# Kernel optimization log

Measured on AMD Instinct MI355X. Metric: run time of the kernel, lower is better.

Reference implementation:

```python
import jax, jax.numpy as jnp
import numpy as np

B = 8192
EPS = 1e-5

def _bn(x):
    # BatchNorm1d(affine=False) in training mode: batch mean, biased variance
    m = x.mean(axis=0)
    v = x.var(axis=0)
    return (x - m) / jnp.sqrt(v + EPS)

def setup_inputs() -> dict:
    key = jax.random.key(0)
    ks = jax.random.split(key, 16)
    sparse_feat = jax.random.randint(ks[0], (B, 26), 0, 1000, dtype=jnp.int32)
    dense_feat = jax.random.normal(ks[1], (B, 13), dtype=jnp.float32)
    emb_a = jax.random.normal(ks[2], (8, 100000, 106), dtype=jnp.float32)
    emb_b = jax.random.normal(ks[3], (10, 10000, 60), dtype=jnp.float32)
    emb_c = jax.random.normal(ks[4], (8, 1000, 33), dtype=jnp.float32)
    F = 8 * 106 + 10 * 60 + 8 * 33 + 13  # 1725
    n_cross = 4  # n_cross_layer + 1
    cross_w = jax.random.normal(ks[5], (n_cross, F), dtype=jnp.float32)
    cross_b = jax.random.normal(ks[6], (n_cross, F), dtype=jnp.float32)
    s = 1.0 / np.sqrt(F)
    W1 = jax.random.uniform(ks[7], (F, 1024), minval=-s, maxval=s, dtype=jnp.float32)
    b1 = jax.random.uniform(ks[8], (1024,), minval=-s, maxval=s, dtype=jnp.float32)
    s = 1.0 / np.sqrt(1024)
    W2 = jax.random.uniform(ks[9], (1024, 512), minval=-s, maxval=s, dtype=jnp.float32)
    b2 = jax.random.uniform(ks[10], (512,), minval=-s, maxval=s, dtype=jnp.float32)
    s = 1.0 / np.sqrt(512)
    W3 = jax.random.uniform(ks[11], (512, 256), minval=-s, maxval=s, dtype=jnp.float32)
    b3 = jax.random.uniform(ks[12], (256,), minval=-s, maxval=s, dtype=jnp.float32)
    s = 1.0 / np.sqrt(F + 256)
    Wout = jax.random.uniform(ks[13], (F + 256, 1), minval=-s, maxval=s, dtype=jnp.float32)
    return {"sparse_feat": sparse_feat, "dense_feat": dense_feat,
            "emb_a": emb_a, "emb_b": emb_b, "emb_c": emb_c,
            "cross_w": cross_w, "cross_b": cross_b,
            "W1": W1, "b1": b1, "W2": W2, "b2": b2, "W3": W3, "b3": b3,
            "Wout": Wout}

def reference(sparse_feat, dense_feat, emb_a, emb_b, emb_c,
              cross_w, cross_b, W1, b1, W2, b2, W3, b3, Wout):
    # multi-embedding gather + concat
    ia = sparse_feat[:, :8]          # (B,8)
    ib = sparse_feat[:, 8:18]        # (B,10)
    ic = sparse_feat[:, 18:26]       # (B,8)
    va = emb_a[jnp.arange(8)[None, :], ia].reshape(ia.shape[0], -1)    # (B, 8*106)
    vb = emb_b[jnp.arange(10)[None, :], ib].reshape(ib.shape[0], -1)   # (B, 10*60)
    vc = emb_c[jnp.arange(8)[None, :], ic].reshape(ic.shape[0], -1)    # (B, 8*33)
    h = jnp.concatenate([va, vb, vc, dense_feat], axis=1)              # (B, F)
    h = _bn(h)
    # CrossNetwork: x_{i+1} = x0 * (x_i . w_i) + b_i + x_i
    # (matmul(x0, x_i^T) @ w_i == x0 * dot(x_i, w_i), same math, O(F) form)
    x0 = h
    xi = h
    for i in range(cross_w.shape[0]):
        xi = x0 * (xi @ cross_w[i])[:, None] + cross_b[i][None, :] + xi
    out_cross = xi                                                     # (B, F)
    # DeepNetwork: Linear -> BN(affine=False) -> ReLU, three layers
    d = jax.nn.relu(_bn(h @ W1 + b1))
    d = jax.nn.relu(_bn(d @ W2 + b2))
    d = jax.nn.relu(_bn(d @ W3 + b3))                                  # (B, 256)
    final = jnp.concatenate([out_cross, d], axis=1)                    # (B, F+256)
    logits = (final @ Wout)[:, 0]
    return jax.nn.sigmoid(logits)
```

## Files before the change

kernel.cpp:

```cpp
#include <hip/hip_runtime.h>
#include <math.h>

#define B 8192
#define FA 848
#define FB 600
#define FC 264
#define ND 13
#define F 1725
#define KP1 1728
#define N1 1024
#define N2 512
#define N3 256
#define EPS 1e-5f

typedef __attribute__((ext_vector_type(4))) float f32x4;
typedef __attribute__((ext_vector_type(8))) short bf16x8;
typedef unsigned short u16;
typedef unsigned int u32;

__device__ __forceinline__ u16 f2bf(float x) {
  u32 b = __builtin_bit_cast(u32, x);
  u32 r = (b + 0x7fffu + ((b >> 16) & 1u)) >> 16;
  return (u16)r;
}
__device__ __forceinline__ float bf2f(u16 h) {
  return __builtin_bit_cast(float, (u32)h << 16);
}

__global__ __launch_bounds__(256) void gather_kernel(
    const int* __restrict__ sparse, const float* __restrict__ dense,
    const float* __restrict__ ea, const float* __restrict__ eb,
    const float* __restrict__ ec, float* __restrict__ h) {
  int r = blockIdx.x;
  const int* sp = sparse + r * 26;
  float* hr = h + (size_t)r * F;
  for (int j = threadIdx.x; j < F; j += 256) {
    float v;
    if (j < FA) {
      int t = j / 106, c = j - t * 106;
      v = ea[(size_t)t * 10600000 + (size_t)sp[t] * 106 + c];
    } else if (j < FA + FB) {
      int jj = j - FA; int t = jj / 60, c = jj - t * 60;
      v = eb[(size_t)t * 600000 + (size_t)sp[8 + t] * 60 + c];
    } else if (j < FA + FB + FC) {
      int jj = j - FA - FB; int t = jj / 33, c = jj - t * 33;
      v = ec[(size_t)t * 33000 + (size_t)sp[18 + t] * 33 + c];
    } else {
      v = dense[r * ND + (j - (FA + FB + FC))];
    }
    hr[j] = v;
  }
}

__global__ __launch_bounds__(256) void colstat_kernel(
    const float* __restrict__ X, int C, float* __restrict__ sums) {
  int j = blockIdx.x * 256 + threadIdx.x;
  if (j >= C) return;
  int rows_per = B / gridDim.y;
  int r0 = blockIdx.y * rows_per;
  int r1 = r0 + rows_per;
  float s = 0.f, ss = 0.f;
  for (int r = r0; r < r1; ++r) {
    float x = X[(size_t)r * C + j];
    s += x; ss += x * x;
  }
  atomicAdd(&sums[j], s);
  atomicAdd(&sums[C + j], ss);
}

__global__ __launch_bounds__(256) void finstat_kernel(
    const float* __restrict__ sums, int C, float* __restrict__ mi) {
  int j = blockIdx.x * 256 + threadIdx.x;
  if (j >= C) return;
  float m = sums[j] * (1.0f / B);
  float v = sums[C + j] * (1.0f / B) - m * m;
  mi[j] = m;
  mi[C + j] = rsqrtf(v + EPS);
}

__global__ __launch_bounds__(256) void bnapply_h_kernel(
    const float* __restrict__ h, const float* __restrict__ mi,
    u32* __restrict__ hbf) {
  int r = blockIdx.x;
  const float* xr = h + (size_t)r * F;
  u32* br = hbf + (size_t)r * (KP1 / 2);
  for (int jj = threadIdx.x; jj < KP1 / 2; jj += 256) {
    int c0 = jj * 2, c1 = c0 + 1;
    float x0 = 0.f, x1 = 0.f;
    if (c0 < F) x0 = (xr[c0] - mi[c0]) * mi[F + c0];
    if (c1 < F) x1 = (xr[c1] - mi[c1]) * mi[F + c1];
    br[jj] = (u32)f2bf(x0) | ((u32)f2bf(x1) << 16);
  }
}

__global__ __launch_bounds__(256) void prep_kernel(
    const float* __restrict__ mi, const float* __restrict__ cw,
    const float* __restrict__ cb, const float* __restrict__ wout,
    float* __restrict__ cwf, float* __restrict__ consts) {
  int tid = threadIdx.x;
  float acc9[9];
#pragma unroll
  for (int q = 0; q < 9; ++q) acc9[q] = 0.f;
  for (int j = tid; j < F; j += 256) {
    float m = mi[j], inv = mi[F + j];
    float w0 = cw[j], w1 = cw[F + j], w2 = cw[2 * F + j], w3 = cw[3 * F + j];
    float w4 = wout[j];
    cwf[j] = inv * w0;          acc9[0] += m * inv * w0;
    cwf[F + j] = inv * w1;      acc9[1] += m * inv * w1;
    cwf[2 * F + j] = inv * w2;  acc9[2] += m * inv * w2;
    cwf[3 * F + j] = inv * w3;  acc9[3] += m * inv * w3;
    cwf[4 * F + j] = inv * w4;  acc9[4] += m * inv * w4;
    float c1 = cb[j];
    float c2 = c1 + cb[F + j];
    float c3 = c2 + cb[2 * F + j];
    float c4 = c3 + cb[3 * F + j];
    acc9[5] += c1 * w1;
    acc9[6] += c2 * w2;
    acc9[7] += c3 * w3;
    acc9[8] += c4 * w4;
  }
  __shared__ float red[9][4];
  int lane = tid & 63, wid = tid >> 6;
#pragma unroll
  for (int q = 0; q < 9; ++q) {
    float v = acc9[q];
    for (int off = 32; off; off >>= 1) v += __shfl_down(v, off, 64);
    if (lane == 0) red[q][wid] = v;
  }
  __syncthreads();
  if (tid == 0) {
    float t[9];
#pragma unroll
    for (int q = 0; q < 9; ++q) t[q] = red[q][0] + red[q][1] + red[q][2] + red[q][3];
    consts[0] = t[0]; consts[1] = t[1]; consts[2] = t[2]; consts[3] = t[3];
    consts[4] = t[4];
    consts[5] = 0.f; consts[6] = t[5]; consts[7] = t[6]; consts[8] = t[7];
    consts[9] = t[8];
  }
}

__global__ __launch_bounds__(256) void gemv_cross_kernel(
    const float* __restrict__ h, const float* __restrict__ cwf,
    const float* __restrict__ consts, float* __restrict__ cpart) {
  int r = blockIdx.x, tid = threadIdx.x;
  const float* hr = h + (size_t)r * F;
  float p[5] = {0.f, 0.f, 0.f, 0.f, 0.f};
  for (int j = tid; j < F; j += 256) {
    float x = hr[j];
    p[0] += x * cwf[j];
    p[1] += x * cwf[F + j];
    p[2] += x * cwf[2 * F + j];
    p[3] += x * cwf[3 * F + j];
    p[4] += x * cwf[4 * F + j];
  }
  __shared__ float red[5][4];
  int lane = tid & 63, wid = tid >> 6;
#pragma unroll
  for (int i = 0; i < 5; ++i) {
    float v = p[i];
    for (int off = 32; off; off >>= 1) v += __shfl_down(v, off, 64);
    if (lane == 0) red[i][wid] = v;
  }
  __syncthreads();
  if (tid == 0) {
    float u[5];
#pragma unroll
    for (int i = 0; i < 5; ++i)
      u[i] = red[i][0] + red[i][1] + red[i][2] + red[i][3] - consts[i];
    float a = 1.f;
#pragma unroll
    for (int i = 0; i < 4; ++i) {
      float s = a * u[i] + consts[5 + i];
      a += s;
    }
    cpart[r] = a * u[4] + consts[9];
  }
}

__global__ __launch_bounds__(256) void convw_kernel(
    const float* __restrict__ W, int K, int N, int Kp, u16* __restrict__ Wt) {
  __shared__ float t[32][33];
  int n0 = blockIdx.x * 32, k0 = blockIdx.y * 32;
  int tx = threadIdx.x, ty = threadIdx.y;
#pragma unroll
  for (int i = 0; i < 4; ++i) {
    int k = k0 + ty + i * 8;
    t[ty + i * 8][tx] = (k < K) ? W[(size_t)k * N + n0 + tx] : 0.f;
  }
  __syncthreads();
#pragma unroll
  for (int i = 0; i < 4; ++i) {
    int n = n0 + ty + i * 8;
    Wt[(size_t)n * Kp + k0 + tx] = f2bf(t[tx][ty + i * 8]);
  }
}

template <bool OUT_BF>
__global__ __launch_bounds__(256) void gemm_bf16_kernel(
    const u16* __restrict__ A, const u16* __restrict__ Bt,
    void* __restrict__ Cout, float* __restrict__ gsum, int N, int K) {
  __shared__ u16 As[128 * 32];
  __shared__ u16 Bs[128 * 32];
  int tid = threadIdx.x;
  int lane = tid & 63;
  int wave = tid >> 6;
  int row0 = blockIdx.y * 128, col0 = blockIdx.x * 128;
  int wm = (wave >> 1) * 64, wn = (wave & 1) * 64;
  int mrow = lane & 15;
  int kq = lane >> 4;

  f32x4 acc[4][4];
#pragma unroll
  for (int i = 0; i < 4; ++i)
#pragma unroll
    for (int j = 0; j < 4; ++j) acc[i][j] = (f32x4){0.f, 0.f, 0.f, 0.f};

  int kc = (tid & 3) * 8;
  const u16* Ag = A + (size_t)row0 * K;
  const u16* Bg = Bt + (size_t)col0 * K;

  for (int k0 = 0; k0 < K; k0 += 32) {
#pragma unroll
    for (int i = 0; i < 2; ++i) {
      int u = i * 256 + tid;
      int rr = u >> 2;
      __builtin_amdgcn_global_load_lds(
          (const __attribute__((address_space(1))) u32*)(Ag + (size_t)rr * K + k0 + kc),
          (__attribute__((address_space(3))) u32*)(As + u * 8), 16, 0, 0);
      __builtin_amdgcn_global_load_lds(
          (const __attribute__((address_space(1))) u32*)(Bg + (size_t)rr * K + k0 + kc),
          (__attribute__((address_space(3))) u32*)(Bs + u * 8), 16, 0, 0);
    }
    __syncthreads();
    bf16x8 af[4], bfr[4];
#pragma unroll
    for (int mi = 0; mi < 4; ++mi)
      af[mi] = *(const bf16x8*)(As + (wm + mi * 16 + mrow) * 32 + kq * 8);
#pragma unroll
    for (int ni = 0; ni < 4; ++ni)
      bfr[ni] = *(const bf16x8*)(Bs + (wn + ni * 16 + mrow) * 32 + kq * 8);
#pragma unroll
    for (int mi = 0; mi < 4; ++mi)
#pragma unroll
      for (int ni = 0; ni < 4; ++ni)
        acc[mi][ni] = __builtin_amdgcn_mfma_f32_16x16x32_bf16(
            af[mi], bfr[ni], acc[mi][ni], 0, 0, 0);
    __syncthreads();
  }

  float* sred = (float*)As;
  sred[tid] = 0.f;
  __syncthreads();
#pragma unroll
  for (int ni = 0; ni < 4; ++ni) {
    int col_l = wn + ni * 16 + mrow;
    int col = col0 + col_l;
    float s = 0.f, ss = 0.f;
#pragma unroll
    for (int mi = 0; mi < 4; ++mi) {
#pragma unroll
      for (int reg = 0; reg < 4; ++reg) {
        int row = row0 + wm + mi * 16 + kq * 4 + reg;
        float v = acc[mi][ni][reg];
        if (OUT_BF) {
          u16 hb = f2bf(v);
          v = bf2f(hb);
          ((u16*)Cout)[(size_t)row * N + col] = hb;
        } else {
          ((float*)Cout)[(size_t)row * N + col] = v;
        }
        s += v;
        ss += v * v;
      }
    }
    s += __shfl_xor(s, 16, 64);  s += __shfl_xor(s, 32, 64);
    ss += __shfl_xor(ss, 16, 64); ss += __shfl_xor(ss, 32, 64);
    if (kq == 0) {
      atomicAdd(&sred[col_l], s);
      atomicAdd(&sred[128 + col_l], ss);
    }
  }
  __syncthreads();
  if (tid < 128) {
    atomicAdd(&gsum[col0 + tid], sred[tid]);
    atomicAdd(&gsum[N + col0 + tid], sred[128 + tid]);
  }
}

__global__ __launch_bounds__(256) void bn_relu_bb_kernel(
    const uint4* __restrict__ X, const float* __restrict__ mi,
    uint4* __restrict__ out, int Cmask, int total8) {
  int i = blockIdx.x * 256 + threadIdx.x;
  if (i >= total8) return;
  uint4 v = X[i];
  int colb = (i << 3) & Cmask;
  int C = Cmask + 1;
  u32 w[4] = {v.x, v.y, v.z, v.w};
  u32 o[4];
#pragma unroll
  for (int e = 0; e < 4; ++e) {
    int c0 = colb + e * 2, c1 = c0 + 1;
    float x0 = bf2f((u16)(w[e] & 0xffffu));
    float x1 = bf2f((u16)(w[e] >> 16));
    x0 = fmaxf((x0 - mi[c0]) * mi[C + c0], 0.f);
    x1 = fmaxf((x1 - mi[c1]) * mi[C + c1], 0.f);
    o[e] = (u32)f2bf(x0) | ((u32)f2bf(x1) << 16);
  }
  out[i] = make_uint4(o[0], o[1], o[2], o[3]);
}

__global__ __launch_bounds__(256) void bn_relu_f32_kernel(
    float* __restrict__ X, int C, const float* __restrict__ mi) {
  int r = blockIdx.x;
  float* xr = X + (size_t)r * C;
  for (int j = threadIdx.x; j < C; j += 256) {
    float x = (xr[j] - mi[j]) * mi[C + j];
    xr[j] = fmaxf(x, 0.f);
  }
}

__global__ __launch_bounds__(256) void final_kernel(
    const float* __restrict__ cpart, const float* __restrict__ d3,
    const float* __restrict__ wout, float* __restrict__ out) {
  int r = blockIdx.x, tid = threadIdx.x;
  float local = d3[(size_t)r * N3 + tid] * wout[F + tid];
  for (int off = 32; off; off >>= 1) local += __shfl_down(local, off, 64);
  __shared__ float red[4];
  int lane = tid & 63, wid = tid >> 6;
  if (lane == 0) red[wid] = local;
  __syncthreads();
  if (tid == 0) {
    float s = cpart[r] + red[0] + red[1] + red[2] + red[3];
    out[r] = 1.0f / (1.0f + expf(-s));
  }
}

extern "C" void kernel_launch(void* const* d_in, const int* in_sizes, int n_in,
                              void* d_out, int out_size, void* d_ws,
                              size_t ws_size, hipStream_t stream) {
  const int* sparse = (const int*)d_in[0];
  const float* dense = (const float*)d_in[1];
  const float* ea = (const float*)d_in[2];
  const float* eb = (const float*)d_in[3];
  const float* ec = (const float*)d_in[4];
  const float* cw = (const float*)d_in[5];
  const float* cb = (const float*)d_in[6];
  const float* W1 = (const float*)d_in[7];
  const float* W2 = (const float*)d_in[9];
  const float* W3 = (const float*)d_in[11];
  const float* Wout = (const float*)d_in[13];
  float* out = (float*)d_out;

  float* ws = (float*)d_ws;
  size_t o = 0;
  float* h = ws + o;      o += (size_t)B * F;
  float* z3 = ws + o;     o += (size_t)B * N3;
  float* cpart = ws + o;  o += B;
  float* sums = ws + o;   o += 4096;
  float* mi = ws + o;     o += 4096;
  float* consts = ws + o; o += 16;
  float* cwf = ws + o;    o += 5 * F + 8;  o = (o + 7) & ~(size_t)7;
  u16* hbf = (u16*)(ws + o);  o += (size_t)B * KP1 / 2;
  u16* z1 = (u16*)(ws + o);   o += (size_t)B * N1 / 2;
  u16* z1n = (u16*)(ws + o);  o += (size_t)B * N1 / 2;
  u16* z2 = (u16*)(ws + o);   o += (size_t)B * N2 / 2;
  u16* z2n = (u16*)(ws + o);  o += (size_t)B * N2 / 2;
  u16* W1t = (u16*)(ws + o);  o += (size_t)N1 * KP1 / 2;
  u16* W2t = (u16*)(ws + o);  o += (size_t)N2 * N1 / 2;
  u16* W3t = (u16*)(ws + o);  o += (size_t)N3 * N2 / 2;

  dim3 tb(32, 8);
  convw_kernel<<<dim3(N1 / 32, KP1 / 32), tb, 0, stream>>>(W1, F, N1, KP1, W1t);
  convw_kernel<<<dim3(N2 / 32, N1 / 32), tb, 0, stream>>>(W2, N1, N2, N1, W2t);
  convw_kernel<<<dim3(N3 / 32, N2 / 32), tb, 0, stream>>>(W3, N2, N3, N2, W3t);

  gather_kernel<<<B, 256, 0, stream>>>(sparse, dense, ea, eb, ec, h);

  hipMemsetAsync(sums, 0, 4096 * sizeof(float), stream);
  colstat_kernel<<<dim3(7, 64), 256, 0, stream>>>(h, F, sums);
  finstat_kernel<<<7, 256, 0, stream>>>(sums, F, mi);

  bnapply_h_kernel<<<B, 256, 0, stream>>>(h, mi, (u32*)hbf);
  prep_kernel<<<1, 256, 0, stream>>>(mi, cw, cb, Wout, cwf, consts);
  gemv_cross_kernel<<<B, 256, 0, stream>>>(h, cwf, consts, cpart);

  hipMemsetAsync(sums, 0, 4096 * sizeof(float), stream);
  gemm_bf16_kernel<true><<<dim3(N1 / 128, B / 128), 256, 0, stream>>>(
      hbf, W1t, (void*)z1, sums, N1, KP1);
  finstat_kernel<<<4, 256, 0, stream>>>(sums, N1, mi);
  bn_relu_bb_kernel<<<(B * N1 / 8 + 255) / 256, 256, 0, stream>>>(
      (const uint4*)z1, mi, (uint4*)z1n, N1 - 1, B * N1 / 8);

  hipMemsetAsync(sums, 0, 4096 * sizeof(float), stream);
  gemm_bf16_kernel<true><<<dim3(N2 / 128, B / 128), 256, 0, stream>>>(
      z1n, W2t, (void*)z2, sums, N2, N1);
  finstat_kernel<<<2, 256, 0, stream>>>(sums, N2, mi);
  bn_relu_bb_kernel<<<(B * N2 / 8 + 255) / 256, 256, 0, stream>>>(
      (const uint4*)z2, mi, (uint4*)z2n, N2 - 1, B * N2 / 8);

  hipMemsetAsync(sums, 0, 4096 * sizeof(float), stream);
  gemm_bf16_kernel<false><<<dim3(N3 / 128, B / 128), 256, 0, stream>>>(
      z2n, W3t, (void*)z3, sums, N3, N2);
  finstat_kernel<<<1, 256, 0, stream>>>(sums, N3, mi);
  bn_relu_f32_kernel<<<B, 256, 0, stream>>>(z3, N3, mi);

  final_kernel<<<B, 256, 0, stream>>>(cpart, z3, Wout, out);
}
```

Before: 646.2 us.

## Fuse BN statistics into gather, merge pipeline kernels and drop finstat launches

Measured after the change: 645.1 us. Within noise of the previous version (-0.2%).

```diff
diff --git a/kernel.cpp b/kernel.cpp
--- a/kernel.cpp
+++ b/kernel.cpp
@@ -12,6 +12,7 @@
 #define N2 512
 #define N3 256
 #define EPS 1e-5f
+#define GROWS 16
 
 typedef __attribute__((ext_vector_type(4))) float f32x4;
 typedef __attribute__((ext_vector_type(8))) short bf16x8;
@@ -27,131 +28,121 @@
   return __builtin_bit_cast(float, (u32)h << 16);
 }
 
-__global__ __launch_bounds__(256) void gather_kernel(
+__global__ __launch_bounds__(256) void gather_stats_kernel(
     const int* __restrict__ sparse, const float* __restrict__ dense,
     const float* __restrict__ ea, const float* __restrict__ eb,
-    const float* __restrict__ ec, float* __restrict__ h) {
-  int r = blockIdx.x;
-  const int* sp = sparse + r * 26;
-  float* hr = h + (size_t)r * F;
-  for (int j = threadIdx.x; j < F; j += 256) {
-    float v;
-    if (j < FA) {
-      int t = j / 106, c = j - t * 106;
-      v = ea[(size_t)t * 10600000 + (size_t)sp[t] * 106 + c];
-    } else if (j < FA + FB) {
-      int jj = j - FA; int t = jj / 60, c = jj - t * 60;
-      v = eb[(size_t)t * 600000 + (size_t)sp[8 + t] * 60 + c];
-    } else if (j < FA + FB + FC) {
-      int jj = j - FA - FB; int t = jj / 33, c = jj - t * 33;
-      v = ec[(size_t)t * 33000 + (size_t)sp[18 + t] * 33 + c];
-    } else {
-      v = dense[r * ND + (j - (FA + FB + FC))];
-    }
-    hr[j] = v;
-  }
-}
-
-__global__ __launch_bounds__(256) void colstat_kernel(
-    const float* __restrict__ X, int C, float* __restrict__ sums) {
-  int j = blockIdx.x * 256 + threadIdx.x;
-  if (j >= C) return;
-  int rows_per = B / gridDim.y;
-  int r0 = blockIdx.y * rows_per;
-  int r1 = r0 + rows_per;
-  float s = 0.f, ss = 0.f;
-  for (int r = r0; r < r1; ++r) {
-    float x = X[(size_t)r * C + j];
-    s += x; ss += x * x;
-  }
-  atomicAdd(&sums[j], s);
-  atomicAdd(&sums[C + j], ss);
-}
-
-__global__ __launch_bounds__(256) void finstat_kernel(
-    const float* __restrict__ sums, int C, float* __restrict__ mi) {
-  int j = blockIdx.x * 256 + threadIdx.x;
-  if (j >= C) return;
-  float m = sums[j] * (1.0f / B);
-  float v = sums[C + j] * (1.0f / B) - m * m;
-  mi[j] = m;
-  mi[C + j] = rsqrtf(v + EPS);
-}
-
-__global__ __launch_bounds__(256) void bnapply_h_kernel(
+    const float* __restrict__ ec, float* __restrict__ h,
+    float* __restrict__ sums) {
+  int r0 = blockIdx.x * GROWS;
+  int tid = threadIdx.x;
+  __shared__ int sp_s[GROWS][26];
+  for (int t = tid; t < GROWS * 26; t += 256)
+    sp_s[t / 26][t % 26] = sparse[(r0 + t / 26) * 26 + t % 26];
+  __syncthreads();
+  float s[7], ss[7];
+#pragma unroll
+  for (int q = 0; q < 7; ++q) { s[q] = 0.f; ss[q] = 0.f; }
+  for (int rr = 0; rr < GROWS; ++rr) {
+    int r = r0 + rr;
+    const int* sp = sp_s[rr];
+    float* hr = h + (size_t)r * F;
+    int it = 0;
+    for (int j = tid; j < F; j += 256, ++it) {
+      float v;
+      if (j < FA) {
+        int t = j / 106, c = j - t * 106;
+        v = ea[(size_t)t * 10600000 + (size_t)sp[t] * 106 + c];
+      } else if (j < FA + FB) {
+        int jj = j - FA; int t = jj / 60, c = jj - t * 60;
+        v = eb[(size_t)t * 600000 + (size_t)sp[8 + t] * 60 + c];
+      } else if (j < FA + FB + FC) {
+        int jj = j - FA - FB; int t = jj / 33, c = jj - t * 33;
+        v = ec[(size_t)t * 33000 + (size_t)sp[18 + t] * 33 + c];
+      } else {
+        v = dense[r * ND + (j - (FA + FB + FC))];
+      }
+      hr[j] = v;
+      s[it] += v; ss[it] += v * v;
+    }
+  }
+#pragma unroll
+  for (int q = 0; q < 7; ++q) {
+    int j = q * 256 + tid;
+    if (j < F) {
+      atomicAdd(&sums[j], s[q]);
+      atomicAdd(&sums[F + j], ss[q]);
+    }
+  }
+}
+
+__global__ __launch_bounds__(256) void prep_kernel(
+    const float* __restrict__ sums, const float* __restrict__ cw,
+    const float* __restrict__ cb, const float* __restrict__ wout,
+    float* __restrict__ mi, float* __restrict__ consts) {
+  int tid = threadIdx.x;
+  float acc[4] = {0.f, 0.f, 0.f, 0.f};
+  for (int j = tid; j < F; j += 256) {
+    float m = sums[j] * (1.0f / B);
+    float v = sums[F + j] * (1.0f / B) - m * m;
+    float inv = rsqrtf(v + EPS);
+    mi[j] = m;
+    mi[F + j] = inv;
+    float c1 = cb[j];
+    float c2 = c1 + cb[F + j];
+    float c3 = c2 + cb[2 * F + j];
+    float c4 = c3 + cb[3 * F + j];
+    acc[0] += c1 * cw[F + j];
+    acc[1] += c2 * cw[2 * F + j];
+    acc[2] += c3 * cw[3 * F + j];
+    acc[3] += c4 * wout[j];
+  }
+  __shared__ float red[4][4];
+  int lane = tid & 63, wid = tid >> 6;
+#pragma unroll
+  for (int q = 0; q < 4; ++q) {
+    float v = acc[q];
+    for (int off = 32; off; off >>= 1) v += __shfl_down(v, off, 64);
+    if (lane == 0) red[q][wid] = v;
+  }
+  __syncthreads();
+  if (tid == 0) {
+    consts[0] = 0.f;
+    consts[1] = red[0][0] + red[0][1] + red[0][2] + red[0][3];
+    consts[2] = red[1][0] + red[1][1] + red[1][2] + red[1][3];
+    consts[3] = red[2][0] + red[2][1] + red[2][2] + red[2][3];
+    consts[4] = red[3][0] + red[3][1] + red[3][2] + red[3][3];
+  }
+}
+
+__global__ __launch_bounds__(256) void bnapply_gemv_kernel(
     const float* __restrict__ h, const float* __restrict__ mi,
-    u32* __restrict__ hbf) {
-  int r = blockIdx.x;
+    const float* __restrict__ cw, const float* __restrict__ wout,
+    const float* __restrict__ consts, u32* __restrict__ hbf,
+    float* __restrict__ cpart) {
+  int r = blockIdx.x, tid = threadIdx.x;
   const float* xr = h + (size_t)r * F;
   u32* br = hbf + (size_t)r * (KP1 / 2);
-  for (int jj = threadIdx.x; jj < KP1 / 2; jj += 256) {
+  float p[5] = {0.f, 0.f, 0.f, 0.f, 0.f};
+  for (int jj = tid; jj < KP1 / 2; jj += 256) {
     int c0 = jj * 2, c1 = c0 + 1;
     float x0 = 0.f, x1 = 0.f;
     if (c0 < F) x0 = (xr[c0] - mi[c0]) * mi[F + c0];
     if (c1 < F) x1 = (xr[c1] - mi[c1]) * mi[F + c1];
     br[jj] = (u32)f2bf(x0) | ((u32)f2bf(x1) << 16);
-  }
-}
-
-__global__ __launch_bounds__(256) void prep_kernel(
-    const float* __restrict__ mi, const float* __restrict__ cw,
-    const float* __restrict__ cb, const float* __restrict__ wout,
-    float* __restrict__ cwf, float* __restrict__ consts) {
-  int tid = threadIdx.x;
-  float acc9[9];
-#pragma unroll
-  for (int q = 0; q < 9; ++q) acc9[q] = 0.f;
-  for (int j = tid; j < F; j += 256) {
-    float m = mi[j], inv = mi[F + j];
-    float w0 = cw[j], w1 = cw[F + j], w2 = cw[2 * F + j], w3 = cw[3 * F + j];
-    float w4 = wout[j];
-    cwf[j] = inv * w0;          acc9[0] += m * inv * w0;
-    cwf[F + j] = inv * w1;      acc9[1] += m * inv * w1;
-    cwf[2 * F + j] = inv * w2;  acc9[2] += m * inv * w2;
-    cwf[3 * F + j] = inv * w3;  acc9[3] += m * inv * w3;
-    cwf[4 * F + j] = inv * w4;  acc9[4] += m * inv * w4;
-    float c1 = cb[j];
-    float c2 = c1 + cb[F + j];
-    float c3 = c2 + cb[2 * F + j];
-    float c4 = c3 + cb[3 * F + j];
-    acc9[5] += c1 * w1;
-    acc9[6] += c2 * w2;
-    acc9[7] += c3 * w3;
-    acc9[8] += c4 * w4;
-  }
-  __shared__ float red[9][4];
-  int lane = tid & 63, wid = tid >> 6;
-#pragma unroll
-  for (int q = 0; q < 9; ++q) {
-    float v = acc9[q];
-    for (int off = 32; off; off >>= 1) v += __shfl_down(v, off, 64);
-    if (lane == 0) red[q][wid] = v;
-  }
-  __syncthreads();
-  if (tid == 0) {
-    float t[9];
-#pragma unroll
-    for (int q = 0; q < 9; ++q) t[q] = red[q][0] + red[q][1] + red[q][2] + red[q][3];
-    consts[0] = t[0]; consts[1] = t[1]; consts[2] = t[2]; consts[3] = t[3];
-    consts[4] = t[4];
-    consts[5] = 0.f; consts[6] = t[5]; consts[7] = t[6]; consts[8] = t[7];
-    consts[9] = t[8];
-  }
-}
-
-__global__ __launch_bounds__(256) void gemv_cross_kernel(
-    const float* __restrict__ h, const float* __restrict__ cwf,
-    const float* __restrict__ consts, float* __restrict__ cpart) {
-  int r = blockIdx.x, tid = threadIdx.x;
-  const float* hr = h + (size_t)r * F;
-  float p[5] = {0.f, 0.f, 0.f, 0.f, 0.f};
-  for (int j = tid; j < F; j += 256) {
-    float x = hr[j];
-    p[0] += x * cwf[j];
-    p[1] += x * cwf[F + j];
-    p[2] += x * cwf[2 * F + j];
-    p[3] += x * cwf[3 * F + j];
-    p[4] += x * cwf[4 * F + j];
+    if (c0 < F) {
+      p[0] += x0 * cw[c0];
+      p[1] += x0 * cw[F + c0];
+      p[2] += x0 * cw[2 * F + c0];
+      p[3] += x0 * cw[3 * F + c0];
+      p[4] += x0 * wout[c0];
+    }
+    if (c1 < F) {
+      p[0] += x1 * cw[c1];
+      p[1] += x1 * cw[F + c1];
+      p[2] += x1 * cw[2 * F + c1];
+      p[3] += x1 * cw[3 * F + c1];
+      p[4] += x1 * wout[c1];
+    }
   }
   __shared__ float red[5][4];
   int lane = tid & 63, wid = tid >> 6;
@@ -166,21 +157,34 @@
     float u[5];
 #pragma unroll
     for (int i = 0; i < 5; ++i)
-      u[i] = red[i][0] + red[i][1] + red[i][2] + red[i][3] - consts[i];
+      u[i] = red[i][0] + red[i][1] + red[i][2] + red[i][3];
     float a = 1.f;
 #pragma unroll
     for (int i = 0; i < 4; ++i) {
-      float s = a * u[i] + consts[5 + i];
-      a += s;
-    }
-    cpart[r] = a * u[4] + consts[9];
-  }
-}
-
-__global__ __launch_bounds__(256) void convw_kernel(
-    const float* __restrict__ W, int K, int N, int Kp, u16* __restrict__ Wt) {
+      float sv = a * u[i] + consts[i];
+      a += sv;
+    }
+    cpart[r] = a * u[4] + consts[4];
+  }
+}
+
+__global__ __launch_bounds__(256) void convw_all_kernel(
+    const float* __restrict__ W1, const float* __restrict__ W2,
+    const float* __restrict__ W3, u16* __restrict__ W1t,
+    u16* __restrict__ W2t, u16* __restrict__ W3t) {
+  int b = blockIdx.x;
+  const float* W; u16* Wt; int K, N, Kp, bx, by;
+  if (b < 1728) {
+    W = W1; Wt = W1t; K = F;  N = N1; Kp = KP1; bx = b & 31; by = b >> 5;
+  } else if (b < 2240) {
+    b -= 1728;
+    W = W2; Wt = W2t; K = N1; N = N2; Kp = N1;  bx = b & 15; by = b >> 4;
+  } else {
+    b -= 2240;
+    W = W3; Wt = W3t; K = N2; N = N3; Kp = N2;  bx = b & 7;  by = b >> 3;
+  }
   __shared__ float t[32][33];
-  int n0 = blockIdx.x * 32, k0 = blockIdx.y * 32;
+  int n0 = bx * 32, k0 = by * 32;
   int tx = threadIdx.x, ty = threadIdx.y;
 #pragma unroll
   for (int i = 0; i < 4; ++i) {
@@ -288,46 +292,44 @@
 }
 
 __global__ __launch_bounds__(256) void bn_relu_bb_kernel(
-    const uint4* __restrict__ X, const float* __restrict__ mi,
+    const uint4* __restrict__ X, const float* __restrict__ sums,
     uint4* __restrict__ out, int Cmask, int total8) {
   int i = blockIdx.x * 256 + threadIdx.x;
   if (i >= total8) return;
   uint4 v = X[i];
   int colb = (i << 3) & Cmask;
   int C = Cmask + 1;
+  const float invB = 1.0f / B;
   u32 w[4] = {v.x, v.y, v.z, v.w};
   u32 o[4];
 #pragma unroll
   for (int e = 0; e < 4; ++e) {
     int c0 = colb + e * 2, c1 = c0 + 1;
+    float m0 = sums[c0] * invB, m1 = sums[c1] * invB;
+    float i0 = rsqrtf(sums[C + c0] * invB - m0 * m0 + EPS);
+    float i1 = rsqrtf(sums[C + c1] * invB - m1 * m1 + EPS);
     float x0 = bf2f((u16)(w[e] & 0xffffu));
     float x1 = bf2f((u16)(w[e] >> 16));
-    x0 = fmaxf((x0 - mi[c0]) * mi[C + c0], 0.f);
-    x1 = fmaxf((x1 - mi[c1]) * mi[C + c1], 0.f);
+    x0 = fmaxf((x0 - m0) * i0, 0.f);
+    x1 = fmaxf((x1 - m1) * i1, 0.f);
     o[e] = (u32)f2bf(x0) | ((u32)f2bf(x1) << 16);
   }
   out[i] = make_uint4(o[0], o[1], o[2], o[3]);
 }
 
-__global__ __launch_bounds__(256) void bn_relu_f32_kernel(
-    float* __restrict__ X, int C, const float* __restrict__ mi) {
-  int r = blockIdx.x;
-  float* xr = X + (size_t)r * C;
-  for (int j = threadIdx.x; j < C; j += 256) {
-    float x = (xr[j] - mi[j]) * mi[C + j];
-    xr[j] = fmaxf(x, 0.f);
-  }
-}
-
 __global__ __launch_bounds__(256) void final_kernel(
-    const float* __restrict__ cpart, const float* __restrict__ d3,
-    const float* __restrict__ wout, float* __restrict__ out) {
+    const float* __restrict__ cpart, const float* __restrict__ z3,
+    const float* __restrict__ sums, const float* __restrict__ wout,
+    float* __restrict__ out) {
   int r = blockIdx.x, tid = threadIdx.x;
-  float local = d3[(size_t)r * N3 + tid] * wout[F + tid];
-  for (int off = 32; off; off >>= 1) local += __shfl_down(local, off, 64);
+  const float invB = 1.0f / B;
+  float m = sums[tid] * invB;
+  float inv = rsqrtf(sums[N3 + tid] * invB - m * m + EPS);
+  float x = fmaxf((z3[(size_t)r * N3 + tid] - m) * inv, 0.f) * wout[F + tid];
+  for (int off = 32; off; off >>= 1) x += __shfl_down(x, off, 64);
   __shared__ float red[4];
   int lane = tid & 63, wid = tid >> 6;
-  if (lane == 0) red[wid] = local;
+  if (lane == 0) red[wid] = x;
   __syncthreads();
   if (tid == 0) {
     float s = cpart[r] + red[0] + red[1] + red[2] + red[3];
@@ -356,10 +358,13 @@
   float* h = ws + o;      o += (size_t)B * F;
   float* z3 = ws + o;     o += (size_t)B * N3;
   float* cpart = ws + o;  o += B;
-  float* sums = ws + o;   o += 4096;
-  float* mi = ws + o;     o += 4096;
-  float* consts = ws + o; o += 16;
-  float* cwf = ws + o;    o += 5 * F + 8;  o = (o + 7) & ~(size_t)7;
+  float* stats = ws + o;  o += 8192;
+  float* sumsF = stats;
+  float* g1 = stats + 3456;
+  float* g2 = stats + 5504;
+  float* g3 = stats + 6528;
+  float* mi = ws + o;     o += 3456;
+  float* consts = ws + o; o += 16;  o = (o + 7) & ~(size_t)7;
   u16* hbf = (u16*)(ws + o);  o += (size_t)B * KP1 / 2;
   u16* z1 = (u16*)(ws + o);   o += (size_t)B * N1 / 2;
   u16* z1n = (u16*)(ws + o);  o += (size_t)B * N1 / 2;
@@ -369,40 +374,28 @@
   u16* W2t = (u16*)(ws + o);  o += (size_t)N2 * N1 / 2;
   u16* W3t = (u16*)(ws + o);  o += (size_t)N3 * N2 / 2;
 
-  dim3 tb(32, 8);
-  convw_kernel<<<dim3(N1 / 32, KP1 / 32), tb, 0, stream>>>(W1, F, N1, KP1, W1t);
-  convw_kernel<<<dim3(N2 / 32, N1 / 32), tb, 0, stream>>>(W2, N1, N2, N1, W2t);
-  convw_kernel<<<dim3(N3 / 32, N2 / 32), tb, 0, stream>>>(W3, N2, N3, N2, W3t);
-
-  gather_kernel<<<B, 256, 0, stream>>>(sparse, dense, ea, eb, ec, h);
-
-  hipMemsetAsync(sums, 0, 4096 * sizeof(float), stream);
-  colstat_kernel<<<dim3(7, 64), 256, 0, stream>>>(h, F, sums);
-  finstat_kernel<<<7, 256, 0, stream>>>(sums, F, mi);
-
-  bnapply_h_kernel<<<B, 256, 0, stream>>>(h, mi, (u32*)hbf);
-  prep_kernel<<<1, 256, 0, stream>>>(mi, cw, cb, Wout, cwf, consts);
-  gemv_cross_kernel<<<B, 256, 0, stream>>>(h, cwf, consts, cpart);
-
-  hipMemsetAsync(sums, 0, 4096 * sizeof(float), stream);
+  hipMemsetAsync(stats, 0, 8192 * sizeof(float), stream);
+
+  convw_all_kernel<<<2368, dim3(32, 8), 0, stream>>>(W1, W2, W3, W1t, W2t, W3t);
+
+  gather_stats_kernel<<<B / GROWS, 256, 0, stream>>>(sparse, dense, ea, eb, ec,
+                                                     h, sumsF);
+  prep_kernel<<<1, 256, 0, stream>>>(sumsF, cw, cb, Wout, mi, consts);
+  bnapply_gemv_kernel<<<B, 256, 0, stream>>>(h, mi, cw, Wout, consts,
+                                             (u32*)hbf, cpart);
+
   gemm_bf16_kernel<true><<<dim3(N1 / 128, B / 128), 256, 0, stream>>>(
-      hbf, W1t, (void*)z1, sums, N1, KP1);
-  finstat_kernel<<<4, 256, 0, stream>>>(sums, N1, mi);
+      hbf, W1t, (void*)z1, g1, N1, KP1);
   bn_relu_bb_kernel<<<(B * N1 / 8 + 255) / 256, 256, 0, stream>>>(
-      (const uint4*)z1, mi, (uint4*)z1n, N1 - 1, B * N1 / 8);
-
-  hipMemsetAsync(sums, 0, 4096 * sizeof(float), stream);
+      (const uint4*)z1, g1, (uint4*)z1n, N1 - 1, B * N1 / 8);
+
   gemm_bf16_kernel<true><<<dim3(N2 / 128, B / 128), 256, 0, stream>>>(
-      z1n, W2t, (void*)z2, sums, N2, N1);
-  finstat_kernel<<<2, 256, 0, stream>>>(sums, N2, mi);
+      z1n, W2t, (void*)z2, g2, N2, N1);
   bn_relu_bb_kernel<<<(B * N2 / 8 + 255) / 256, 256, 0, stream>>>(
-      (const uint4*)z2, mi, (uint4*)z2n, N2 - 1, B * N2 / 8);
-
-  hipMemsetAsync(sums, 0, 4096 * sizeof(float), stream);
+      (const uint4*)z2, g2, (uint4*)z2n, N2 - 1, B * N2 / 8);
+
   gemm_bf16_kernel<false><<<dim3(N3 / 128, B / 128), 256, 0, stream>>>(
-      z2n, W3t, (void*)z3, sums, N3, N2);
-  finstat_kernel<<<1, 256, 0, stream>>>(sums, N3, mi);
-  bn_relu_f32_kernel<<<B, 256, 0, stream>>>(z3, N3, mi);
-
-  final_kernel<<<B, 256, 0, stream>>>(cpart, z3, Wout, out);
-}
+      z2n, W3t, (void*)z3, g3, N3, N2);
+
+  final_kernel<<<B, 256, 0, stream>>>(cpart, z3, g3, Wout, out);
+}
```
